# Performance work log

Hardware: AMD Instinct MI355X
Metric: run time of the kernel (lower is better)

The kernel has to match this reference:

```python
import jax, jax.numpy as jnp
import numpy as np
from jax import lax

N_SUBJ = 4096
N_STEPS = 2048
N_DOSES = 8
T_HOURS = 504.0  # 21 days
BASELINE_R = 16.0


def setup_inputs() -> dict:
    key = jax.random.key(0)
    k1, k2, k3, k4, k5 = jax.random.split(key, 5)
    # covariates: body weight ~ U[50,100] kg, comed status in [0,1)
    bw = 50.0 + 50.0 * jax.random.uniform(k1, (N_SUBJ,), dtype=jnp.float32)
    comed = jax.random.uniform(k2, (N_SUBJ,), dtype=jnp.float32)
    cov = jnp.stack([bw, comed], axis=1)  # [N,2]
    dose_intensity = jax.random.uniform(k3, (N_SUBJ,), dtype=jnp.float32)
    # surrogate param_estimator weights: linear map [bw_norm, comed, dose] -> 9 params
    W = 0.5 * jax.random.normal(k4, (3, 9), dtype=jnp.float32)
    b = jax.random.normal(k5, (9,), dtype=jnp.float32)
    # per-subject dose amounts for each of the N_DOSES events (mg, ~[0,20))
    dose_amounts = 20.0 * jax.random.uniform(jax.random.fold_in(key, 7), (N_SUBJ, N_DOSES), dtype=jnp.float32)
    return {"cov": cov, "dose_intensity": dose_intensity, "W": W, "b": b, "dose_amounts": dose_amounts}


def _ode_rhs(y, P):
    # y: [N,4]; P: tuple of 9 arrays each [N]
    Ka, CL, Vc, Q, Vp, Kin, Kout, Imax, IC50 = P
    A_d, A_c, A_p, R = y[:, 0], y[:, 1], y[:, 2], y[:, 3]
    dA_d = -Ka * A_d
    dA_c = Ka * A_d - (CL / Vc) * A_c - (Q / Vc) * A_c + (Q / Vp) * A_p
    dA_p = (Q / Vc) * A_c - (Q / Vp) * A_p
    conc = A_c / Vc
    inhibition = Imax * conc / (IC50 + conc + 1e-6)
    dR = Kin * (1.0 - inhibition) - Kout * R
    return jnp.stack([dA_d, dA_c, dA_p, dR], axis=-1)


def reference(cov, dose_intensity, W, b, dose_amounts):
    N = cov.shape[0]
    dt = jnp.float32(T_HOURS / N_STEPS)
    # param estimator surrogate: (covariates, dose intensity) -> 9 positive PK/PD params
    feats = jnp.concatenate([cov * jnp.array([0.01, 1.0], jnp.float32), dose_intensity[:, None]], axis=1)  # [N,3]
    params = jax.nn.softplus(feats @ W + b) + 0.01  # [N,9], strictly positive
    P = tuple(params[:, i] for i in range(9))

    # discrete dose events: dose k added to depot at step k*steps_per_dose
    steps_per_dose = N_STEPS // N_DOSES
    dose_steps = jnp.arange(N_DOSES) * steps_per_dose  # [N_DOSES]
    dose_add = jnp.zeros((N_STEPS, N), params.dtype).at[dose_steps].set(dose_amounts.T)  # [T,N]

    y0 = jnp.concatenate([jnp.zeros((N, 3), params.dtype), jnp.full((N, 1), BASELINE_R, params.dtype)], axis=1)

    def step(y, dose):
        # discrete dosing: bolus into depot compartment (state index 0)
        y = y.at[:, 0].add(dose)
        k1 = _ode_rhs(y, P)
        k2 = _ode_rhs(y + 0.5 * dt * k1, P)
        k3 = _ode_rhs(y + 0.5 * dt * k2, P)
        k4 = _ode_rhs(y + dt * k3, P)
        y_new = y + (dt / 6.0) * (k1 + 2.0 * k2 + 2.0 * k3 + k4)
        return y_new, y_new

    _, traj = lax.scan(step, y0, dose_add)  # [T,N,4]
    out = jnp.concatenate([y0[None], traj], axis=0)  # [T+1,N,4]
    return jnp.transpose(out, (1, 0, 2))  # [N, T+1, 4]
```

## Files before the change

kernel.cpp:

```cpp
#include <hip/hip_runtime.h>

#define N_SUBJ 4096
#define N_STEPS 2048
#define N_DOSES 8

#define DT   0.24609375f

__device__ __forceinline__ float softplusf(float x) {
    return fmaxf(x, 0.0f) + log1pf(expf(-fabsf(x)));
}

__device__ __forceinline__ void mm3(float* C, const float* A, const float* B) {
#pragma unroll
    for (int i = 0; i < 3; ++i)
#pragma unroll
        for (int j = 0; j < 3; ++j)
            C[3 * i + j] = A[3 * i] * B[j] + A[3 * i + 1] * B[3 + j] + A[3 * i + 2] * B[6 + j];
}

#define DPPF(v, ctrl, rmask) __int_as_float(__builtin_amdgcn_update_dpp( \
        0, __float_as_int(v), (ctrl), (rmask), 0xf, true))

__device__ __forceinline__ float rfl(float x) {
    return __int_as_float(__builtin_amdgcn_readfirstlane(__float_as_int(x)));
}

__global__ __launch_bounds__(256, 4) void pkpd_tint_kernel(
    const float* __restrict__ cov,
    const float* __restrict__ dose_int,
    const float* __restrict__ Wm,
    const float* __restrict__ bvec,
    const float* __restrict__ dose_amt,
    float* __restrict__ out)
{
    const int c = threadIdx.x & 63;
    const int subj = blockIdx.x * 4 + (threadIdx.x >> 6);

    const float f0 = cov[2 * subj] * 0.01f;
    const float f1 = cov[2 * subj + 1];
    const float f2 = dose_int[subj];

    float P[9];
#pragma unroll
    for (int p = 0; p < 9; ++p) {
        float z = f0 * Wm[p] + f1 * Wm[9 + p] + f2 * Wm[18 + p] + bvec[p];
        P[p] = softplusf(z) + 0.01f;
    }
    const float Ka = P[0], CL = P[1], Vc = P[2], Q_ = P[3], Vp = P[4];
    const float Kin = P[5], Kout = P[6], Imax = P[7], IC50 = P[8];

    const float k10 = CL / Vc, k12 = Q_ / Vc, k21 = Q_ / Vp;
    const float IC50p = IC50 + 1e-6f;

    const float x = DT * Kout;
    const float x2 = x * x;
    const float alpha = 1.0f - x + 0.5f * x2 - (1.0f / 6.0f) * x2 * x + (1.0f / 24.0f) * x2 * x2;
    const float a = 0.5f * x;
    const float g1 = 1.0f - 2.0f * a + 2.0f * a * a - 2.0f * a * a * a;
    const float g2 = 2.0f - 2.0f * a + 2.0f * a * a;
    const float g3 = 2.0f - 2.0f * a;
    const float s0 = DT * Kin * (1.0f / 6.0f);
    const float w1 = s0 * g1, w2 = s0 * g2, w3 = s0 * g3, w4 = s0;
    const float beta0v = w1 + w2 + w3 + w4;

    float Am[9] = { -DT * Ka, 0.0f, 0.0f,
                     DT * Ka, -DT * (k10 + k12), DT * k21,
                     0.0f, DT * k12, -DT * k21 };
    float S2[9], S3[9], S4[9], G[9], Phi[9];
#pragma unroll
    for (int e = 0; e < 9; ++e) S2[e] = 0.5f * Am[e];
    S2[0] += 1.0f; S2[4] += 1.0f; S2[8] += 1.0f;
    mm3(S3, Am, S2);
#pragma unroll
    for (int e = 0; e < 9; ++e) S3[e] = 0.5f * S3[e];
    S3[0] += 1.0f; S3[4] += 1.0f; S3[8] += 1.0f;
    mm3(S4, Am, S3);
    S4[0] += 1.0f; S4[4] += 1.0f; S4[8] += 1.0f;
#pragma unroll
    for (int e = 0; e < 9; ++e) G[e] = 2.0f * (S2[e] + S3[e]) + S4[e];
    G[0] += 1.0f; G[4] += 1.0f; G[8] += 1.0f;
    mm3(Phi, Am, G);
#pragma unroll
    for (int e = 0; e < 9; ++e) Phi[e] *= (1.0f / 6.0f);
    Phi[0] += 1.0f; Phi[4] += 1.0f; Phi[8] += 1.0f;

    float Pc[9], Tm[9];
#pragma unroll
    for (int e = 0; e < 9; ++e) Pc[e] = Phi[e];
    float v0 = 1.0f, v1 = 0.0f, v2 = 0.0f;
    if (c & 1) { v0 = Pc[0]; v1 = Pc[3]; v2 = Pc[6]; }
#pragma unroll
    for (int bb = 1; bb <= 5; ++bb) {
        mm3(Tm, Pc, Pc);
#pragma unroll
        for (int e = 0; e < 9; ++e) Pc[e] = Tm[e];
        float tv0 = Pc[0] * v0 + Pc[1] * v1 + Pc[2] * v2;
        float tv1 = Pc[3] * v0 + Pc[4] * v1 + Pc[5] * v2;
        float tv2 = Pc[6] * v0 + Pc[7] * v1 + Pc[8] * v2;
        const bool bit = (c >> bb) & 1;
        v0 = bit ? tv0 : v0; v1 = bit ? tv1 : v1; v2 = bit ? tv2 : v2;
    }
    mm3(Tm, Pc, Pc);

    float sPhi[9], sF64[9], sU[9];
#pragma unroll
    for (int e = 0; e < 9; ++e) {
        sPhi[e] = rfl(Phi[e]);
        sF64[e] = rfl(Tm[e]);
    }
    sU[0] = rfl(S2[3]); sU[1] = rfl(S2[4]); sU[2] = rfl(S2[5]);
    sU[3] = rfl(S3[3]); sU[4] = rfl(S3[4]); sU[5] = rfl(S3[5]);
    sU[6] = rfl(S4[3]); sU[7] = rfl(S4[4]); sU[8] = rfl(S4[5]);
    const float sD    = rfl(IC50p * Vc);
    const float sWW1  = rfl(w1 * Imax);
    const float sWW2  = rfl(w2 * Imax);
    const float sWW3  = rfl(w3 * Imax);
    const float sWW4  = rfl(w4 * Imax);
    const float sB0   = rfl(beta0v);

    const float a1 = alpha, a2 = a1 * a1, a4 = a2 * a2;
    const float a8 = a4 * a4, a16 = a8 * a8, a32 = a16 * a16;
    float pca = alpha;
    pca *= (c & 1)  ? a1  : 1.0f;
    pca *= (c & 2)  ? a2  : 1.0f;
    pca *= (c & 4)  ? a4  : 1.0f;
    pca *= (c & 8)  ? a8  : 1.0f;
    pca *= (c & 16) ? a16 : 1.0f;
    pca *= (c & 32) ? a32 : 1.0f;
    float w5 = alpha;
    w5 *= (c & 1) ? a1 : 1.0f;
    w5 *= (c & 2) ? a2 : 1.0f;
    w5 *= (c & 4) ? a4 : 1.0f;
    w5 *= (c & 8) ? a8 : 1.0f;
    float w6 = w5 * ((c & 16) ? a16 : 1.0f);

    const float4 dlo = ((const float4*)(dose_amt + subj * N_DOSES))[0];
    const float4 dhi = ((const float4*)(dose_amt + subj * N_DOSES))[1];
    const float ds[8] = { dlo.x, dlo.y, dlo.z, dlo.w, dhi.x, dhi.y, dhi.z, dhi.w };

    float x0 = ds[0] * v0, x1d = ds[0] * v1, x2d = ds[0] * v2;
    float Rc = 16.0f;

    float4* orow = (float4*)out + (size_t)subj * (N_STEPS + 1);
    if (c == 0) orow[0] = make_float4(0.0f, 0.0f, 0.0f, 16.0f);
    float4* op = orow + 1 + c;

#define BETA_FROM_X(bout)                                                  \
    do {                                                                   \
        float s1_ = x1d;                                                   \
        float s2_ = sU[0] * x0 + sU[1] * x1d + sU[2] * x2d;                \
        float s3_ = sU[3] * x0 + sU[4] * x1d + sU[5] * x2d;                \
        float s4_ = sU[6] * x0 + sU[7] * x1d + sU[8] * x2d;                \
        float d1_ = sD + s1_, d2_ = sD + s2_;                              \
        float d3_ = sD + s3_, d4_ = sD + s4_;                              \
        float n12_ = fmaf(sWW1 * s1_, d2_, (sWW2 * s2_) * d1_);            \
        float n34_ = fmaf(sWW3 * s3_, d4_, (sWW4 * s4_) * d3_);            \
        float d12_ = d1_ * d2_, d34_ = d3_ * d4_;                          \
        float num_ = fmaf(n12_, d34_, n34_ * d12_);                        \
        float rcp_ = __builtin_amdgcn_rcpf(d12_ * d34_);                   \
        bout = sB0 - num_ * rcp_;                                          \
    } while (0)

    float bta;
    BETA_FROM_X(bta);

#pragma unroll
    for (int k = 0; k < 32; ++k) {
        float xn0 = sPhi[0] * x0 + sPhi[1] * x1d + sPhi[2] * x2d;
        float xn1 = sPhi[3] * x0 + sPhi[4] * x1d + sPhi[5] * x2d;
        float xn2 = sPhi[6] * x0 + sPhi[7] * x1d + sPhi[8] * x2d;

        float I = bta;
        I = fmaf(a1, DPPF(I, 0x111, 0xf), I);
        I = fmaf(a2, DPPF(I, 0x112, 0xf), I);
        I = fmaf(a4, DPPF(I, 0x114, 0xf), I);
        I = fmaf(a8, DPPF(I, 0x118, 0xf), I);
        I = fmaf(w5, DPPF(I, 0x142, 0xa), I);
        I = fmaf(w6, DPPF(I, 0x143, 0xc), I);

        if (k < 31) {
            float nx0 = sF64[0] * x0 + sF64[1] * x1d + sF64[2] * x2d;
            float nx1 = sF64[3] * x0 + sF64[4] * x1d + sF64[5] * x2d;
            float nx2 = sF64[6] * x0 + sF64[7] * x1d + sF64[8] * x2d;
            if ((k & 3) == 3) {
                const float dd = ds[(k >> 2) + 1];
                nx0 = fmaf(dd, v0, nx0);
                nx1 = fmaf(dd, v1, nx1);
                nx2 = fmaf(dd, v2, nx2);
            }
            x0 = nx0; x1d = nx1; x2d = nx2;
            BETA_FROM_X(bta);
        }

        float Rout = fmaf(pca, Rc, I);
        op[k * 64] = make_float4(xn0, xn1, xn2, Rout);

        Rc = __int_as_float(__builtin_amdgcn_readlane(__float_as_int(Rout), 63));
    }
#undef BETA_FROM_X
}

extern "C" void kernel_launch(void* const* d_in, const int* in_sizes, int n_in,
                              void* d_out, int out_size, void* d_ws, size_t ws_size,
                              hipStream_t stream) {
    const float* cov      = (const float*)d_in[0];
    const float* dose_int = (const float*)d_in[1];
    const float* Wm       = (const float*)d_in[2];
    const float* bvec     = (const float*)d_in[3];
    const float* dose_amt = (const float*)d_in[4];
    float* out = (float*)d_out;

    pkpd_tint_kernel<<<N_SUBJ / 4, 256, 0, stream>>>(cov, dose_int, Wm, bvec, dose_amt, out);
}
```

Measured before the change: 32.65 us.

## Split each subject across two wavefronts with redundant prefix recompute

Each subject is now handled by two wavefronts. One writes the first 24 rounds of output; the other recomputes those rounds without storing them, then writes the last 8 rounds. This doubles the number of waves to spread the store-bound work and raises the launch-bounds occupancy target. The cost is redundant arithmetic in the second wave, which still runs the full serial chain, and a longer critical path per subject. Alpha powers are also made wave-uniform with readfirstlane, and dose amounts are loaded per segment instead of up front.

```diff
diff --git a/kernel.cpp b/kernel.cpp
--- a/kernel.cpp
+++ b/kernel.cpp
@@ -25,7 +25,7 @@
     return __int_as_float(__builtin_amdgcn_readfirstlane(__float_as_int(x)));
 }
 
-__global__ __launch_bounds__(256, 4) void pkpd_tint_kernel(
+__global__ __launch_bounds__(256, 8) void pkpd_split_kernel(
     const float* __restrict__ cov,
     const float* __restrict__ dose_int,
     const float* __restrict__ Wm,
@@ -34,7 +34,9 @@
     float* __restrict__ out)
 {
     const int c = threadIdx.x & 63;
-    const int subj = blockIdx.x * 4 + (threadIdx.x >> 6);
+    const int g = blockIdx.x * 4 + (threadIdx.x >> 6);
+    const int subj = g >> 1;
+    const int role = g & 1;
 
     const float f0 = cov[2 * subj] * 0.01f;
     const float f1 = cov[2 * subj + 1];
@@ -118,31 +120,30 @@
     const float sWW4  = rfl(w4 * Imax);
     const float sB0   = rfl(beta0v);
 
-    const float a1 = alpha, a2 = a1 * a1, a4 = a2 * a2;
-    const float a8 = a4 * a4, a16 = a8 * a8, a32 = a16 * a16;
-    float pca = alpha;
-    pca *= (c & 1)  ? a1  : 1.0f;
-    pca *= (c & 2)  ? a2  : 1.0f;
-    pca *= (c & 4)  ? a4  : 1.0f;
-    pca *= (c & 8)  ? a8  : 1.0f;
-    pca *= (c & 16) ? a16 : 1.0f;
-    pca *= (c & 32) ? a32 : 1.0f;
-    float w5 = alpha;
-    w5 *= (c & 1) ? a1 : 1.0f;
-    w5 *= (c & 2) ? a2 : 1.0f;
-    w5 *= (c & 4) ? a4 : 1.0f;
-    w5 *= (c & 8) ? a8 : 1.0f;
-    float w6 = w5 * ((c & 16) ? a16 : 1.0f);
-
-    const float4 dlo = ((const float4*)(dose_amt + subj * N_DOSES))[0];
-    const float4 dhi = ((const float4*)(dose_amt + subj * N_DOSES))[1];
-    const float ds[8] = { dlo.x, dlo.y, dlo.z, dlo.w, dhi.x, dhi.y, dhi.z, dhi.w };
-
-    float x0 = ds[0] * v0, x1d = ds[0] * v1, x2d = ds[0] * v2;
+    const float a1v = alpha, a2v = a1v * a1v, a4v = a2v * a2v;
+    const float a8v = a4v * a4v, a16v = a8v * a8v, a32v = a16v * a16v;
+    const float sA1 = rfl(a1v), sA2 = rfl(a2v), sA4 = rfl(a4v), sA8 = rfl(a8v);
+
+    float pca = a1v;
+    pca *= (c & 1)  ? a1v  : 1.0f;
+    pca *= (c & 2)  ? a2v  : 1.0f;
+    pca *= (c & 4)  ? a4v  : 1.0f;
+    pca *= (c & 8)  ? a8v  : 1.0f;
+    pca *= (c & 16) ? a16v : 1.0f;
+    pca *= (c & 32) ? a32v : 1.0f;
+    float w5 = a1v;
+    w5 *= (c & 1) ? a1v : 1.0f;
+    w5 *= (c & 2) ? a2v : 1.0f;
+    w5 *= (c & 4) ? a4v : 1.0f;
+    w5 *= (c & 8) ? a8v : 1.0f;
+    float w6 = w5 * ((c & 16) ? a16v : 1.0f);
+
+    const float dose0 = dose_amt[subj * N_DOSES + 0];
+    float x0 = dose0 * v0, x1d = dose0 * v1, x2d = dose0 * v2;
     float Rc = 16.0f;
 
     float4* orow = (float4*)out + (size_t)subj * (N_STEPS + 1);
-    if (c == 0) orow[0] = make_float4(0.0f, 0.0f, 0.0f, 16.0f);
+    if (role == 0 && c == 0) orow[0] = make_float4(0.0f, 0.0f, 0.0f, 16.0f);
     float4* op = orow + 1 + c;
 
 #define BETA_FROM_X(bout)                                                  \
@@ -161,42 +162,61 @@
         bout = sB0 - num_ * rcp_;                                          \
     } while (0)
 
+#define ROUND(SEG, J, FULL)                                                \
+    do {                                                                   \
+        float xn0, xn1, xn2;                                               \
+        if (FULL) {                                                        \
+            xn0 = sPhi[0] * x0 + sPhi[1] * x1d + sPhi[2] * x2d;            \
+            xn1 = sPhi[3] * x0 + sPhi[4] * x1d + sPhi[5] * x2d;            \
+            xn2 = sPhi[6] * x0 + sPhi[7] * x1d + sPhi[8] * x2d;            \
+        }                                                                  \
+        float I = bta;                                                     \
+        I = fmaf(sA1, DPPF(I, 0x111, 0xf), I);             \
+        I = fmaf(sA2, DPPF(I, 0x112, 0xf), I);             \
+        I = fmaf(sA4, DPPF(I, 0x114, 0xf), I);             \
+        I = fmaf(sA8, DPPF(I, 0x118, 0xf), I);             \
+        I = fmaf(w5, DPPF(I, 0x142, 0xa), I);     \
+        I = fmaf(w6, DPPF(I, 0x143, 0xc), I);     \
+        float nx0 = sF64[0] * x0 + sF64[1] * x1d + sF64[2] * x2d;          \
+        float nx1 = sF64[3] * x0 + sF64[4] * x1d + sF64[5] * x2d;          \
+        float nx2 = sF64[6] * x0 + sF64[7] * x1d + sF64[8] * x2d;          \
+        if ((J) == 3) {                                                    \
+            nx0 = fmaf(dnext, v0, nx0);                                    \
+            nx1 = fmaf(dnext, v1, nx1);                                    \
+            nx2 = fmaf(dnext, v2, nx2);                                    \
+        }                                                                  \
+        x0 = nx0; x1d = nx1; x2d = nx2;                                    \
+        BETA_FROM_X(bta);                                                  \
+        float Rout = fmaf(pca, Rc, I);                                     \
+        if (FULL) op[((SEG) * 4 + (J)) * 64] = make_float4(xn0, xn1, xn2, Rout); \
+        Rc = __int_as_float(__builtin_amdgcn_readlane(__float_as_int(Rout), 63)); \
+    } while (0)
+
     float bta;
     BETA_FROM_X(bta);
 
-#pragma unroll
-    for (int k = 0; k < 32; ++k) {
-        float xn0 = sPhi[0] * x0 + sPhi[1] * x1d + sPhi[2] * x2d;
-        float xn1 = sPhi[3] * x0 + sPhi[4] * x1d + sPhi[5] * x2d;
-        float xn2 = sPhi[6] * x0 + sPhi[7] * x1d + sPhi[8] * x2d;
-
-        float I = bta;
-        I = fmaf(a1, DPPF(I, 0x111, 0xf), I);
-        I = fmaf(a2, DPPF(I, 0x112, 0xf), I);
-        I = fmaf(a4, DPPF(I, 0x114, 0xf), I);
-        I = fmaf(a8, DPPF(I, 0x118, 0xf), I);
-        I = fmaf(w5, DPPF(I, 0x142, 0xa), I);
-        I = fmaf(w6, DPPF(I, 0x143, 0xc), I);
-
-        if (k < 31) {
-            float nx0 = sF64[0] * x0 + sF64[1] * x1d + sF64[2] * x2d;
-            float nx1 = sF64[3] * x0 + sF64[4] * x1d + sF64[5] * x2d;
-            float nx2 = sF64[6] * x0 + sF64[7] * x1d + sF64[8] * x2d;
-            if ((k & 3) == 3) {
-                const float dd = ds[(k >> 2) + 1];
-                nx0 = fmaf(dd, v0, nx0);
-                nx1 = fmaf(dd, v1, nx1);
-                nx2 = fmaf(dd, v2, nx2);
-            }
-            x0 = nx0; x1d = nx1; x2d = nx2;
-            BETA_FROM_X(bta);
+    if (role == 0) {
+#pragma unroll 1
+        for (int seg = 0; seg < 6; ++seg) {
+            const float dnext = dose_amt[subj * N_DOSES + seg + 1];
+            ROUND(seg, 0, true); ROUND(seg, 1, true);
+            ROUND(seg, 2, true); ROUND(seg, 3, true);
         }
-
-        float Rout = fmaf(pca, Rc, I);
-        op[k * 64] = make_float4(xn0, xn1, xn2, Rout);
-
-        Rc = __int_as_float(__builtin_amdgcn_readlane(__float_as_int(Rout), 63));
-    }
+    } else {
+#pragma unroll 1
+        for (int seg = 0; seg < 6; ++seg) {
+            const float dnext = dose_amt[subj * N_DOSES + seg + 1];
+            ROUND(seg, 0, false); ROUND(seg, 1, false);
+            ROUND(seg, 2, false); ROUND(seg, 3, false);
+        }
+#pragma unroll 1
+        for (int seg = 6; seg < 8; ++seg) {
+            const float dnext = (seg < 7) ? dose_amt[subj * N_DOSES + seg + 1] : 0.0f;
+            ROUND(seg, 0, true); ROUND(seg, 1, true);
+            ROUND(seg, 2, true); ROUND(seg, 3, true);
+        }
+    }
+#undef ROUND
 #undef BETA_FROM_X
 }
 
@@ -210,5 +230,5 @@
     const float* dose_amt = (const float*)d_in[4];
     float* out = (float*)d_out;
 
-    pkpd_tint_kernel<<<N_SUBJ / 4, 256, 0, stream>>>(cov, dose_int, Wm, bvec, dose_amt, out);
-}
+    pkpd_split_kernel<<<N_SUBJ * 2 / 4, 256, 0, stream>>>(cov, dose_int, Wm, bvec, dose_amt, out);
+}
```

Result: slower. 51.11 us (+56.5%).

## Store pre-step state per lane to drop per-step Phi matvec and shorten R chain

Applied to the files above, without the earlier changes.

Each lane now writes the state at its own step index instead of the state one step later. This removes the per-iteration 3x3 Phi matrix-vector product. The R output comes from an exclusive scan, obtained by subtracting the lane's own term and scaling by 1/alpha. The carried R value advances with a separate alpha^64 multiply-add, which takes the output computation off the cross-lane carry chain. Scan coefficients are moved to wave-uniform scalars, and the first and last rows get special handling (dose subtraction on lane 0, a final store from lane 63). The trade-off is a reciprocal-based rescaling, which can change rounding slightly, on a kernel that is likely limited by output bandwidth.

```diff
diff --git a/kernel.cpp b/kernel.cpp
--- a/kernel.cpp
+++ b/kernel.cpp
@@ -118,21 +118,25 @@
     const float sWW4  = rfl(w4 * Imax);
     const float sB0   = rfl(beta0v);
 
-    const float a1 = alpha, a2 = a1 * a1, a4 = a2 * a2;
-    const float a8 = a4 * a4, a16 = a8 * a8, a32 = a16 * a16;
-    float pca = alpha;
-    pca *= (c & 1)  ? a1  : 1.0f;
-    pca *= (c & 2)  ? a2  : 1.0f;
-    pca *= (c & 4)  ? a4  : 1.0f;
-    pca *= (c & 8)  ? a8  : 1.0f;
-    pca *= (c & 16) ? a16 : 1.0f;
-    pca *= (c & 32) ? a32 : 1.0f;
-    float w5 = alpha;
-    w5 *= (c & 1) ? a1 : 1.0f;
-    w5 *= (c & 2) ? a2 : 1.0f;
-    w5 *= (c & 4) ? a4 : 1.0f;
-    w5 *= (c & 8) ? a8 : 1.0f;
-    float w6 = w5 * ((c & 16) ? a16 : 1.0f);
+    const float a1v = alpha, a2v = a1v * a1v, a4v = a2v * a2v;
+    const float a8v = a4v * a4v, a16v = a8v * a8v, a32v = a16v * a16v;
+    const float sA1 = rfl(a1v), sA2 = rfl(a2v), sA4 = rfl(a4v), sA8 = rfl(a8v);
+    const float sA64  = rfl(a32v * a32v);
+    const float sInvA = rfl(1.0f / alpha);
+
+    float pcaC = 1.0f;
+    pcaC *= (c & 1)  ? a1v  : 1.0f;
+    pcaC *= (c & 2)  ? a2v  : 1.0f;
+    pcaC *= (c & 4)  ? a4v  : 1.0f;
+    pcaC *= (c & 8)  ? a8v  : 1.0f;
+    pcaC *= (c & 16) ? a16v : 1.0f;
+    pcaC *= (c & 32) ? a32v : 1.0f;
+    float w5 = a1v;
+    w5 *= (c & 1) ? a1v : 1.0f;
+    w5 *= (c & 2) ? a2v : 1.0f;
+    w5 *= (c & 4) ? a4v : 1.0f;
+    w5 *= (c & 8) ? a8v : 1.0f;
+    float w6 = w5 * ((c & 16) ? a16v : 1.0f);
 
     const float4 dlo = ((const float4*)(dose_amt + subj * N_DOSES))[0];
     const float4 dhi = ((const float4*)(dose_amt + subj * N_DOSES))[1];
@@ -142,8 +146,7 @@
     float Rc = 16.0f;
 
     float4* orow = (float4*)out + (size_t)subj * (N_STEPS + 1);
-    if (c == 0) orow[0] = make_float4(0.0f, 0.0f, 0.0f, 16.0f);
-    float4* op = orow + 1 + c;
+    float4* op = orow + c;
 
 #define BETA_FROM_X(bout)                                                  \
     do {                                                                   \
@@ -166,17 +169,23 @@
 
 #pragma unroll
     for (int k = 0; k < 32; ++k) {
-        float xn0 = sPhi[0] * x0 + sPhi[1] * x1d + sPhi[2] * x2d;
-        float xn1 = sPhi[3] * x0 + sPhi[4] * x1d + sPhi[5] * x2d;
-        float xn2 = sPhi[6] * x0 + sPhi[7] * x1d + sPhi[8] * x2d;
-
         float I = bta;
-        I = fmaf(a1, DPPF(I, 0x111, 0xf), I);
-        I = fmaf(a2, DPPF(I, 0x112, 0xf), I);
-        I = fmaf(a4, DPPF(I, 0x114, 0xf), I);
-        I = fmaf(a8, DPPF(I, 0x118, 0xf), I);
+        I = fmaf(sA1, DPPF(I, 0x111, 0xf), I);
+        I = fmaf(sA2, DPPF(I, 0x112, 0xf), I);
+        I = fmaf(sA4, DPPF(I, 0x114, 0xf), I);
+        I = fmaf(sA8, DPPF(I, 0x118, 0xf), I);
         I = fmaf(w5, DPPF(I, 0x142, 0xa), I);
         I = fmaf(w6, DPPF(I, 0x143, 0xc), I);
+
+        float E = (I - bta) * sInvA;
+        float Rst = fmaf(pcaC, Rc, E);
+
+        float st0 = x0;
+        if ((k & 3) == 0) { if (c == 0) st0 = x0 - ds[k >> 2]; }
+        op[k * 64] = make_float4(st0, x1d, x2d, Rst);
+
+        float I63 = __int_as_float(__builtin_amdgcn_readlane(__float_as_int(I), 63));
+        Rc = fmaf(sA64, Rc, I63);
 
         if (k < 31) {
             float nx0 = sF64[0] * x0 + sF64[1] * x1d + sF64[2] * x2d;
@@ -191,11 +200,13 @@
             x0 = nx0; x1d = nx1; x2d = nx2;
             BETA_FROM_X(bta);
         }
-
-        float Rout = fmaf(pca, Rc, I);
-        op[k * 64] = make_float4(xn0, xn1, xn2, Rout);
-
-        Rc = __int_as_float(__builtin_amdgcn_readlane(__float_as_int(Rout), 63));
+    }
+
+    {
+        float xf0 = sPhi[0] * x0 + sPhi[1] * x1d + sPhi[2] * x2d;
+        float xf1 = sPhi[3] * x0 + sPhi[4] * x1d + sPhi[5] * x2d;
+        float xf2 = sPhi[6] * x0 + sPhi[7] * x1d + sPhi[8] * x2d;
+        if (c == 63) orow[N_STEPS] = make_float4(xf0, xf1, xf2, Rc);
     }
 #undef BETA_FROM_X
 }
```

Measured after the change: 33.64 us. 3.0% more time.
